# Optimization experiments

Hardware: AMD Instinct MI355X
Metric: run time of the kernel (lower is better)

Reference implementation:

```python
import jax, jax.numpy as jnp
import numpy as np

N, M, D = 8192, 8192, 64
_LIM = 36.0

def _softplus(x):
    # LogexpTransformation.inverse_transform: x if x > 36 else log1p(exp(x))
    return jnp.where(x > _LIM, x, jnp.log1p(jnp.exp(jnp.minimum(x, _LIM))))

def setup_inputs() -> dict:
    key = jax.random.key(0)
    k1, k2, k3 = jax.random.split(key, 3)
    X = jax.random.normal(k1, (N, D), dtype=jnp.float32)
    Z = jax.random.normal(k2, (M, D), dtype=jnp.float32)
    l_raw = jax.random.uniform(k3, (D,), dtype=jnp.float32)
    sigma_f_raw = jnp.ones((), dtype=jnp.float32)
    return {"X": X, "Z": Z, "l_raw": l_raw, "sigma_f_raw": sigma_f_raw}

def reference(X, Z, l_raw, sigma_f_raw):
    l = _softplus(l_raw)                     # [D] length scales
    sigma_f = _softplus(sigma_f_raw)         # scalar signal variance
    inv_length = 1.0 / (l * l)               # [D]
    w = jnp.sqrt(inv_length)                 # scale features instead of [N,M,D] broadcast
    Xs = X * w                               # [N,D]
    Zs = Z * w                               # [M,D]
    # sum_d inv_length[d]*(X-Z)^2 = |Xs|^2 + |Zs|^2 - 2 Xs.Zs  (GEMM-expansion)
    x2 = jnp.sum(Xs * Xs, axis=1)            # [N]
    z2 = jnp.sum(Zs * Zs, axis=1)            # [M]
    cross = Xs @ Zs.T                        # [N,M]
    dist = x2[:, None] + z2[None, :] - 2.0 * cross
    return sigma_f * jnp.exp(-0.5 * dist)
```

## Files before the change

### kernel.cpp

```cpp
#include <hip/hip_runtime.h>
#include <hip/hip_bf16.h>

#define NROWS 8192
#define MCOLS 8192
#define DK    64

typedef _Float16 f16x8 __attribute__((ext_vector_type(8)));
typedef __attribute__((ext_vector_type(8))) short bf16x8;
typedef __attribute__((ext_vector_type(4))) float f32x4;

#define WS_XH 0u
#define WS_ZH (1u << 20)
#define WS_HX (2u << 20)
#define WS_HZ ((2u << 20) + 32768u)
#define WS_NEED ((size_t)(2u << 20) + 65536u)

__device__ __forceinline__ float softplus_f(float x) {
    return x > 36.0f ? x : log1pf(expf(fminf(x, 36.0f)));
}

__global__ void rbf_prep(const float* __restrict__ X, const float* __restrict__ Z,
                         const float* __restrict__ lraw, char* __restrict__ ws) {
    __shared__ float wsc[DK];
    if (threadIdx.x < DK) wsc[threadIdx.x] = 1.0f / softplus_f(lraw[threadIdx.x]);
    __syncthreads();

    int tid = blockIdx.x * 256 + threadIdx.x;
    bool isZ = tid >= 65536;
    int t = tid & 65535;
    int row = t >> 3;
    int kc = t & 7;
    const float* src = (isZ ? Z : X) + (size_t)row * DK + kc * 8;
    float4 v0 = *(const float4*)(src);
    float4 v1 = *(const float4*)(src + 4);
    float f[8] = {v0.x, v0.y, v0.z, v0.w, v1.x, v1.y, v1.z, v1.w};
    f16x8 hv;
    float sq = 0.0f;
    #pragma unroll
    for (int j = 0; j < 8; ++j) {
        _Float16 h = (_Float16)(f[j] * wsc[kc * 8 + j]);
        hv[j] = h;
        float hf = (float)h;
        sq += hf * hf;
    }
    sq += __shfl_xor(sq, 1);
    sq += __shfl_xor(sq, 2);
    sq += __shfl_xor(sq, 4);
    *(f16x8*)(ws + (isZ ? WS_ZH : WS_XH) + (size_t)row * 128 + kc * 16) = hv;
    if (kc == 0) {
        float* nrm = (float*)(ws + (isZ ? WS_HZ : WS_HX));
        nrm[row] = 0.5f * sq;
    }
}

__launch_bounds__(512, 4)
__global__ void rbf_main(const float* __restrict__ sraw, const char* __restrict__ ws,
                         float* __restrict__ out) {
    __shared__ __align__(16) char smem[32768];

    int bid = blockIdx.x;
    int s = (bid & 7) * 512 + (bid >> 3);
    int tR = s >> 6, tC = s & 63;

    const int tid = threadIdx.x;
    const float sf = softplus_f(sraw[0]);

    #pragma unroll
    for (int c = 0; c < 4; ++c) {
        int o = c * 8192 + tid * 16;
        bool isB = o >= 16384;
        int oo = o & 16383;
        int row = oo >> 7;
        int colb = oo & 127;
        const char* src = ws + (isB ? WS_ZH : WS_XH)
                        + (size_t)((isB ? tC : tR) * 128 + row) * 128 + colb;
        float4 v = *(const float4*)(src);
        int dst = (isB ? 16384 : 0) + row * 128 + (colb ^ ((row & 7) << 4));
        *(float4*)(smem + dst) = v;
    }
    __syncthreads();

    const int lane = tid & 63;
    const int wid  = tid >> 6;
    const int wr = wid >> 1;
    const int wc = wid & 1;
    const int lr = lane & 15;
    const int lg = lane >> 4;
    const int swz = (lr & 7) << 4;

    f32x4 acc[2][4];
    #pragma unroll
    for (int a = 0; a < 2; ++a)
        #pragma unroll
        for (int b = 0; b < 4; ++b) acc[a][b] = f32x4{0.f, 0.f, 0.f, 0.f};

    #pragma unroll
    for (int ks = 0; ks < 2; ++ks) {
        int kb = ((lg * 16 + ks * 64) ^ swz);
        f16x8 af[2], bfr[4];
        #pragma unroll
        for (int mi = 0; mi < 2; ++mi)
            af[mi] = *(const f16x8*)(smem + (wr * 32 + mi * 16 + lr) * 128 + kb);
        #pragma unroll
        for (int ni = 0; ni < 4; ++ni)
            bfr[ni] = *(const f16x8*)(smem + 16384 + (wc * 64 + ni * 16 + lr) * 128 + kb);
        #pragma unroll
        for (int mi = 0; mi < 2; ++mi)
            #pragma unroll
            for (int ni = 0; ni < 4; ++ni)
                acc[mi][ni] = __builtin_amdgcn_mfma_f32_16x16x32_f16(
                    af[mi], bfr[ni], acc[mi][ni], 0, 0, 0);
    }

    const float* hx = (const float*)(ws + WS_HX);
    const float* hz = (const float*)(ws + WS_HZ);
    #pragma unroll
    for (int mi = 0; mi < 2; ++mi) {
        int grow0 = tR * 128 + wr * 32 + mi * 16 + lg * 4;
        float4 hxv = *(const float4*)(hx + grow0);
        float hxa[4] = {hxv.x, hxv.y, hxv.z, hxv.w};
        #pragma unroll
        for (int ni = 0; ni < 4; ++ni) {
            int gcol = tC * 128 + wc * 64 + ni * 16 + lr;
            float hzv = hz[gcol];
            size_t obase = (size_t)grow0 * MCOLS + gcol;
            #pragma unroll
            for (int j = 0; j < 4; ++j)
                out[obase + (size_t)j * MCOLS] = sf * __expf(acc[mi][ni][j] - hxa[j] - hzv);
        }
    }
}

__launch_bounds__(512, 4)
__global__ void rbf_fused(const float* __restrict__ X, const float* __restrict__ Z,
                          const float* __restrict__ lraw, const float* __restrict__ sraw,
                          float* __restrict__ out) {
    __shared__ __align__(16) char smem[65536];
    __shared__ float hxz[256];
    __shared__ float wsc[DK];
    __shared__ float sigf_s;

    const int tid = threadIdx.x;
    const int tR = blockIdx.y;
    const int tC = blockIdx.x;

    if (tid < DK) wsc[tid] = 1.0f / softplus_f(lraw[tid]);
    if (tid == 511) sigf_s = softplus_f(sraw[0]);
    __syncthreads();

    #pragma unroll
    for (int i = 0; i < 4; ++i) {
        int rfull = i * 64 + (tid >> 3);
        int r = rfull & 127;
        int kc = tid & 7;
        bool isB = rfull >= 128;
        const float* src = isB ? (Z + (size_t)(tC * 128 + r) * DK + kc * 8)
                               : (X + (size_t)(tR * 128 + r) * DK + kc * 8);
        float4 v0 = *(const float4*)(src);
        float4 v1 = *(const float4*)(src + 4);
        float f[8] = {v0.x, v0.y, v0.z, v0.w, v1.x, v1.y, v1.z, v1.w};
        bf16x8 hv, lv;
        float sq = 0.0f;
        #pragma unroll
        for (int j = 0; j < 8; ++j) {
            float fv = f[j] * wsc[kc * 8 + j];
            sq += fv * fv;
            unsigned int u = __float_as_uint(fv);
            u += 0x7fffu + ((u >> 16) & 1u);
            unsigned short h = (unsigned short)(u >> 16);
            hv[j] = (short)h;
            float hf = __uint_as_float(((unsigned int)h) << 16);
            unsigned int u2 = __float_as_uint(fv - hf);
            u2 += 0x7fffu + ((u2 >> 16) & 1u);
            lv[j] = (short)(unsigned short)(u2 >> 16);
        }
        sq += __shfl_xor(sq, 1);
        sq += __shfl_xor(sq, 2);
        sq += __shfl_xor(sq, 4);
        if (kc == 0) hxz[rfull] = 0.5f * sq;
        int halfOff = isB ? 32768 : 0;
        int byteOff = r * 128 + ((kc * 16) ^ ((r & 7) << 4));
        *(bf16x8*)(smem + halfOff + byteOff) = hv;
        *(bf16x8*)(smem + halfOff + 16384 + byteOff) = lv;
    }
    __syncthreads();

    const int lane = tid & 63;
    const int wid  = tid >> 6;
    const int wr = wid >> 1;
    const int wc = wid & 1;
    const int lr = lane & 15;
    const int lg = lane >> 4;
    const int swz = (lr & 7) << 4;

    f32x4 acc[2][4];
    #pragma unroll
    for (int a = 0; a < 2; ++a)
        #pragma unroll
        for (int b = 0; b < 4; ++b) acc[a][b] = f32x4{0.f, 0.f, 0.f, 0.f};

    #pragma unroll
    for (int pass = 0; pass < 3; ++pass) {
        const char* Ap = smem + ((pass == 2) ? 16384 : 0);
        const char* Bp = smem + 32768 + ((pass == 1) ? 16384 : 0);
        #pragma unroll
        for (int ks = 0; ks < 2; ++ks) {
            int kb = ((lg * 16 + ks * 64) ^ swz);
            bf16x8 af[2], bfr[4];
            #pragma unroll
            for (int mi = 0; mi < 2; ++mi)
                af[mi] = *(const bf16x8*)(Ap + (wr * 32 + mi * 16 + lr) * 128 + kb);
            #pragma unroll
            for (int ni = 0; ni < 4; ++ni)
                bfr[ni] = *(const bf16x8*)(Bp + (wc * 64 + ni * 16 + lr) * 128 + kb);
            #pragma unroll
            for (int mi = 0; mi < 2; ++mi)
                #pragma unroll
                for (int ni = 0; ni < 4; ++ni)
                    acc[mi][ni] = __builtin_amdgcn_mfma_f32_16x16x32_bf16(
                        af[mi], bfr[ni], acc[mi][ni], 0, 0, 0);
        }
    }

    const float sf = sigf_s;
    #pragma unroll
    for (int mi = 0; mi < 2; ++mi) {
        int row0 = wr * 32 + mi * 16 + lg * 4;
        #pragma unroll
        for (int ni = 0; ni < 4; ++ni) {
            int col = wc * 64 + ni * 16 + lr;
            float hzv = hxz[128 + col];
            size_t obase = (size_t)(tR * 128 + row0) * MCOLS + (size_t)(tC * 128 + col);
            #pragma unroll
            for (int j = 0; j < 4; ++j) {
                float arg = acc[mi][ni][j] - (hxz[row0 + j] + hzv);
                out[obase + (size_t)j * MCOLS] = sf * __expf(arg);
            }
        }
    }
}

extern "C" void kernel_launch(void* const* d_in, const int* in_sizes, int n_in,
                              void* d_out, int out_size, void* d_ws, size_t ws_size,
                              hipStream_t stream) {
    const float* X = (const float*)d_in[0];
    const float* Z = (const float*)d_in[1];
    const float* l = (const float*)d_in[2];
    const float* s = (const float*)d_in[3];
    float* out = (float*)d_out;
    if (ws_size >= WS_NEED && d_ws != nullptr) {
        char* ws = (char*)d_ws;
        rbf_prep<<<512, 256, 0, stream>>>(X, Z, l, ws);
        rbf_main<<<4096, 512, 0, stream>>>(s, ws, out);
    } else {
        dim3 grid(MCOLS / 128, NROWS / 128);
        rbf_fused<<<grid, dim3(512), 0, stream>>>(X, Z, l, s, out);
    }
}
```

Measured before the change: 58.43 us.

## Fold log2e and sigma_f into prep, swap MFMA operands for float4 stores

Scales the features by sqrt(log2 e) and folds log2(sigma_f) into the Z norm term, so the epilogue becomes a single raw exp2 with no multiply. Swapping the MFMA A/B operands transposes the accumulator layout so each lane holds 4 consecutive output columns, which allows 16-byte float4 stores in place of scattered scalar stores. This targets the store-bound epilogue writing the 256MB output. The fp16 scaling changes slightly, and subtracting log2(sigma_f) in fp32 could shift precision a little.

```diff
diff --git a/kernel.cpp b/kernel.cpp
--- a/kernel.cpp
+++ b/kernel.cpp
@@ -1,5 +1,6 @@
 #include <hip/hip_runtime.h>
 #include <hip/hip_bf16.h>
+#include <math.h>
 
 #define NROWS 8192
 #define MCOLS 8192
@@ -15,14 +16,18 @@
 #define WS_HZ ((2u << 20) + 32768u)
 #define WS_NEED ((size_t)(2u << 20) + 65536u)
 
+#define SQRT_L2E 1.2011224087864498f
+
 __device__ __forceinline__ float softplus_f(float x) {
     return x > 36.0f ? x : log1pf(expf(fminf(x, 36.0f)));
 }
 
 __global__ void rbf_prep(const float* __restrict__ X, const float* __restrict__ Z,
-                         const float* __restrict__ lraw, char* __restrict__ ws) {
+                         const float* __restrict__ lraw, const float* __restrict__ sraw,
+                         char* __restrict__ ws) {
     __shared__ float wsc[DK];
-    if (threadIdx.x < DK) wsc[threadIdx.x] = 1.0f / softplus_f(lraw[threadIdx.x]);
+    if (threadIdx.x < DK)
+        wsc[threadIdx.x] = SQRT_L2E / softplus_f(lraw[threadIdx.x]);
     __syncthreads();
 
     int tid = blockIdx.x * 256 + threadIdx.x;
@@ -49,13 +54,14 @@
     *(f16x8*)(ws + (isZ ? WS_ZH : WS_XH) + (size_t)row * 128 + kc * 16) = hv;
     if (kc == 0) {
         float* nrm = (float*)(ws + (isZ ? WS_HZ : WS_HX));
-        nrm[row] = 0.5f * sq;
+        float v = 0.5f * sq;
+        if (isZ) v -= log2f(softplus_f(sraw[0]));
+        nrm[row] = v;
     }
 }
 
 __launch_bounds__(512, 4)
-__global__ void rbf_main(const float* __restrict__ sraw, const char* __restrict__ ws,
-                         float* __restrict__ out) {
+__global__ void rbf_main(const char* __restrict__ ws, float* __restrict__ out) {
     __shared__ __align__(16) char smem[32768];
 
     int bid = blockIdx.x;
@@ -63,7 +69,6 @@
     int tR = s >> 6, tC = s & 63;
 
     const int tid = threadIdx.x;
-    const float sf = softplus_f(sraw[0]);
 
     #pragma unroll
     for (int c = 0; c < 4; ++c) {
@@ -109,24 +114,26 @@
             #pragma unroll
             for (int ni = 0; ni < 4; ++ni)
                 acc[mi][ni] = __builtin_amdgcn_mfma_f32_16x16x32_f16(
-                    af[mi], bfr[ni], acc[mi][ni], 0, 0, 0);
+                    bfr[ni], af[mi], acc[mi][ni], 0, 0, 0);
     }
 
     const float* hx = (const float*)(ws + WS_HX);
     const float* hz = (const float*)(ws + WS_HZ);
     #pragma unroll
     for (int mi = 0; mi < 2; ++mi) {
-        int grow0 = tR * 128 + wr * 32 + mi * 16 + lg * 4;
-        float4 hxv = *(const float4*)(hx + grow0);
-        float hxa[4] = {hxv.x, hxv.y, hxv.z, hxv.w};
+        int xrow = tR * 128 + wr * 32 + mi * 16 + lr;
+        float hxv = hx[xrow];
+        size_t rbase = (size_t)xrow * MCOLS;
         #pragma unroll
         for (int ni = 0; ni < 4; ++ni) {
-            int gcol = tC * 128 + wc * 64 + ni * 16 + lr;
-            float hzv = hz[gcol];
-            size_t obase = (size_t)grow0 * MCOLS + gcol;
-            #pragma unroll
-            for (int j = 0; j < 4; ++j)
-                out[obase + (size_t)j * MCOLS] = sf * __expf(acc[mi][ni][j] - hxa[j] - hzv);
+            int zc0 = tC * 128 + wc * 64 + ni * 16 + lg * 4;
+            float4 hzv = *(const float4*)(hz + zc0);
+            float4 o;
+            o.x = __builtin_amdgcn_exp2f(acc[mi][ni][0] - hxv - hzv.x);
+            o.y = __builtin_amdgcn_exp2f(acc[mi][ni][1] - hxv - hzv.y);
+            o.z = __builtin_amdgcn_exp2f(acc[mi][ni][2] - hxv - hzv.z);
+            o.w = __builtin_amdgcn_exp2f(acc[mi][ni][3] - hxv - hzv.w);
+            *(float4*)(out + rbase + zc0) = o;
         }
     }
 }
@@ -250,8 +257,8 @@
     float* out = (float*)d_out;
     if (ws_size >= WS_NEED && d_ws != nullptr) {
         char* ws = (char*)d_ws;
-        rbf_prep<<<512, 256, 0, stream>>>(X, Z, l, ws);
-        rbf_main<<<4096, 512, 0, stream>>>(s, ws, out);
+        rbf_prep<<<512, 256, 0, stream>>>(X, Z, l, s, ws);
+        rbf_main<<<4096, 512, 0, stream>>>(ws, out);
     } else {
         dim3 grid(MCOLS / 128, NROWS / 128);
         rbf_fused<<<grid, dim3(512), 0, stream>>>(X, Z, l, s, out);
```

Result: slower. 63.78 us (+9.1%).
